# Kernel tuning notes

Hardware: AMD Instinct MI355X
Metric: run time of the kernel (lower is better)

Reference implementation:

```python
import math
import jax, jax.numpy as jnp
import numpy as np

B, C, H, W = 16, 128, 128, 128  # width == dim required by nn.LayerNorm(dim) on (b,c,h,w)
HEADS, DIM_HEAD = 8, 32
INNER = HEADS * DIM_HEAD


def _ln_last(x, g, b, eps=1e-5):
    # torch nn.LayerNorm over the LAST axis (here: width), biased variance
    mu = x.mean(-1, keepdims=True)
    var = x.var(-1, keepdims=True)
    return (x - mu) * jax.lax.rsqrt(var + eps) * g + b


def setup_inputs() -> dict:
    key = jax.random.key(0)
    k0, k1, k2 = jax.random.split(key, 3)
    return {
        "fmap": jax.random.normal(k0, (B, C, H, W), jnp.float32),
        "ln0_g": jnp.ones((C,), jnp.float32),
        "ln0_b": jnp.zeros((C,), jnp.float32),
        "w_qkv": jax.random.normal(k1, (3 * INNER, C), jnp.float32) * 0.05,
        "w_out": jax.random.normal(k2, (C, INNER), jnp.float32) * 0.05,
        "ln1_g": jnp.ones((C,), jnp.float32),
        "ln1_b": jnp.zeros((C,), jnp.float32),
    }


def reference(fmap, ln0_g, ln0_b, w_qkv, w_out, ln1_g, ln1_b):
    b, c, x, y = fmap.shape
    n = x * y
    scale = DIM_HEAD ** -0.5

    fm = _ln_last(fmap, ln0_g, ln0_b)
    # 1x1 conv (no bias) == channel matmul
    qkv = jnp.einsum('bcxy,oc->boxy', fm, w_qkv)  # (b, 3*inner, x, y)
    q, k, v = jnp.split(qkv, 3, axis=1)

    def to_heads(t):
        # b (h c) x y -> (b h) (x y) c
        return t.reshape(b, HEADS, DIM_HEAD, n).transpose(0, 1, 3, 2).reshape(b * HEADS, n, DIM_HEAD)

    q, k, v = map(to_heads, (q, k, v))

    q = jax.nn.softmax(q, axis=-1) * scale
    k = jax.nn.softmax(k, axis=-2)
    # l2norm(v) along feature dim (F.normalize, eps=1e-12)
    v = v / jnp.clip(jnp.linalg.norm(v, axis=-1, keepdims=True), 1e-12)
    inv = 1.0 / math.sqrt(n)
    k = k * inv
    v = v * inv

    context = jnp.einsum('bnd,bne->bde', k, v)   # small (d=32, e=32) context
    out = jnp.einsum('bnd,bde->bne', q, context)

    # (b h) (x y) d -> b (h d) x y
    out = out.reshape(b, HEADS, n, DIM_HEAD).transpose(0, 1, 3, 2).reshape(b, INNER, x, y)
    out = jax.nn.gelu(out, approximate=False)  # torch nn.GELU default (erf)
    out = jnp.einsum('bcxy,oc->boxy', out, w_out)  # 1x1 conv, no bias
    return _ln_last(out, ln1_g, ln1_b)
```

## Files before the change

### kernel.cpp

```cpp
#include <hip/hip_runtime.h>
#include <math.h>

#define OFF_MU    0u
#define OFF_RSTD  262144u
#define OFF_CTXA  655360u
#define OFF_CTXS  2818048u
#define OFF_WSPL  2949120u
#define OFF_WQSPL 3047424u
#define OFF_WOSPL 3096576u

typedef __attribute__((ext_vector_type(8))) short bf16x8;
typedef __attribute__((ext_vector_type(4))) float f32x4;

__global__ void prep_kernel(const float* __restrict__ wqkv,
                            const float* __restrict__ wout,
                            float* __restrict__ ws) {
  int idx = blockIdx.x * 256 + threadIdx.x;
  float v;
  unsigned short* wp;
  unsigned plane, slot;
  if (idx < 65536) {
    int row = idx >> 7, c = idx & 127;
    int blk = row >> 7, ol = row & 127;
    int hh = (ol >> 5) & 1;
    int src = ((ol & 64) ? 512 : 256) + (2 * blk + hh) * 32 + (ol & 31);
    v = wqkv[src * 128 + c];
    wp = (unsigned short*)(ws + OFF_WSPL);
    plane = 65536; slot = (unsigned)idx;
  } else if (idx < 98304) {
    int j = idx - 65536;
    v = wqkv[j];
    wp = (unsigned short*)(ws + OFF_WQSPL);
    plane = 32768; slot = (unsigned)j;
  } else {
    int j = idx - 98304;
    v = wout[j];
    wp = (unsigned short*)(ws + OFF_WOSPL);
    plane = 32768; slot = (unsigned)j;
  }
  unsigned int u = __float_as_uint(v);
  float r1 = v - __uint_as_float(u & 0xffff0000u);
  unsigned int u1 = __float_as_uint(r1);
  float r2 = r1 - __uint_as_float(u1 & 0xffff0000u);
  unsigned int u2 = __float_as_uint(r2);
  wp[slot]             = (unsigned short)(u >> 16);
  wp[plane + slot]     = (unsigned short)(u1 >> 16);
  wp[2 * plane + slot] = (unsigned short)(u2 >> 16);
}

__global__ void ln0_stats_kernel(const float* __restrict__ fmap,
                                 float* __restrict__ ws) {
  const int wid = threadIdx.x >> 6, lane = threadIdx.x & 63;
  const int row = blockIdx.x * 4 + wid;
  const float* p = fmap + (size_t)row * 128;
  float a0 = p[lane], a1 = p[lane + 64];
  double s = (double)a0 + (double)a1;
  double q = (double)a0 * a0 + (double)a1 * a1;
  #pragma unroll
  for (int off = 32; off; off >>= 1) {
    s += __shfl_xor(s, off);
    q += __shfl_xor(q, off);
  }
  if (lane == 0) {
    double mu = s * (1.0 / 128.0);
    double var = q * (1.0 / 128.0) - mu * mu;
    ws[OFF_MU + row] = (float)mu;
    ws[OFF_RSTD + row] = (float)(1.0 / sqrt(var + 1e-5));
  }
}

__launch_bounds__(512, 4)
__global__ void kv_ctx_kernel(const float* __restrict__ fmap,
                              const float* __restrict__ g0,
                              const float* __restrict__ b0,
                              float* __restrict__ ws) {
  __shared__ float sm[13888];
  const int x = blockIdx.x, b = blockIdx.y, t = threadIdx.x;
  const int wave = t >> 6, lane = t & 63;
  const int ln = lane & 15, kb = lane >> 4;
  const int or2 = wave >> 1, yc = wave & 1;
  const int dt = lane >> 3, et = lane & 7;
  const int xg = x >> 3;

  float* pb  = sm;
  float* vb  = sm + 2304;
  float* vss = sm + 4608;
  float* ser = sm + 4864;
  float* rnS = sm + 5120;
  float* red = sm + 5184;
  float* pls = sm + 5184;
  float* muS = sm + 13376;
  float* rsS = sm + 13504;
  float* g0S = sm + 13632;
  float* b0S = sm + 13760;
  float* fmS = sm;

  if (t < 128) {
    muS[t] = ws[OFF_MU + (unsigned)((b * 128 + t) * 128 + x)];
    rsS[t] = ws[OFF_RSTD + (unsigned)((b * 128 + t) * 128 + x)];
  } else if (t < 256) g0S[t - 128] = g0[t - 128];
  else if (t < 384) b0S[t - 256] = b0[t - 256];

  const unsigned short* wspl = (const unsigned short*)(ws + OFF_WSPL);

  for (int blk = 0; blk < 4; ++blk) {
    f32x4 acc[2][4];
    #pragma unroll
    for (int i = 0; i < 2; ++i)
      #pragma unroll
      for (int j = 0; j < 4; ++j) acc[i][j] = (f32x4){0.f, 0.f, 0.f, 0.f};

    for (int cc = 0; cc < 4; ++cc) {
      bf16x8 af[2][3];
      #pragma unroll
      for (int ot = 0; ot < 2; ++ot)
        #pragma unroll
        for (int p = 0; p < 3; ++p)
          af[ot][p] = *(const bf16x8*)(wspl + p * 65536 +
              ((blk * 128 + or2 * 32 + ot * 16 + ln) * 128 + cc * 32 + kb * 8));

      __syncthreads();
      #pragma unroll
      for (int it = 0; it < 2; ++it) {
        int idx4 = it * 512 + t;
        int c = idx4 >> 5, y4 = (idx4 & 31) * 4;
        int cg = cc * 32 + c;
        const float4 r = *(const float4*)(fmap + (((size_t)(b * 128 + cg)) * 128 + x) * 128 + y4);
        float mu = muS[cg], rs = rsS[cg];
        float4 g = *(const float4*)(g0S + y4);
        float4 be = *(const float4*)(b0S + y4);
        float4 o;
        o.x = (r.x - mu) * rs * g.x + be.x;
        o.y = (r.y - mu) * rs * g.y + be.y;
        o.z = (r.z - mu) * rs * g.z + be.z;
        o.w = (r.w - mu) * rs * g.w + be.w;
        *(float4*)(fmS + c * 128 + y4) = o;
      }
      __syncthreads();
      {
        const int ty = t & 127, cg = t >> 7;
        unsigned int d0[4], d1[4], d2[4];
        #pragma unroll
        for (int jj = 0; jj < 4; ++jj) {
          unsigned int h[2], m[2], l[2];
          #pragma unroll
          for (int e = 0; e < 2; ++e) {
            float v = fmS[(cg * 8 + jj * 2 + e) * 128 + ty];
            unsigned int u = __float_as_uint(v);
            float r1 = v - __uint_as_float(u & 0xffff0000u);
            unsigned int u1 = __float_as_uint(r1);
            float r2 = r1 - __uint_as_float(u1 & 0xffff0000u);
            h[e] = u >> 16; m[e] = u1 >> 16; l[e] = __float_as_uint(r2) >> 16;
          }
          d0[jj] = h[0] | (h[1] << 16);
          d1[jj] = m[0] | (m[1] << 16);
          d2[jj] = l[0] | (l[1] << 16);
        }
        float* pp = pls + ty * 20 + cg * 4;
        *reinterpret_cast<uint4*>(pp)        = make_uint4(d0[0], d0[1], d0[2], d0[3]);
        *reinterpret_cast<uint4*>(pp + 2560) = make_uint4(d1[0], d1[1], d1[2], d1[3]);
        *reinterpret_cast<uint4*>(pp + 5120) = make_uint4(d2[0], d2[1], d2[2], d2[3]);
      }
      __syncthreads();
      #pragma unroll
      for (int yt = 0; yt < 4; ++yt) {
        const float* bp = pls + ((yc * 4 + yt) * 16 + ln) * 20 + kb * 4;
        bf16x8 B0 = *(const bf16x8*)(bp);
        bf16x8 B1 = *(const bf16x8*)(bp + 2560);
        bf16x8 B2 = *(const bf16x8*)(bp + 5120);
        #pragma unroll
        for (int ot = 0; ot < 2; ++ot) {
          f32x4 c = acc[ot][yt];
          c = __builtin_amdgcn_mfma_f32_16x16x32_bf16(af[ot][0], B0, c, 0, 0, 0);
          c = __builtin_amdgcn_mfma_f32_16x16x32_bf16(af[ot][0], B1, c, 0, 0, 0);
          c = __builtin_amdgcn_mfma_f32_16x16x32_bf16(af[ot][1], B0, c, 0, 0, 0);
          c = __builtin_amdgcn_mfma_f32_16x16x32_bf16(af[ot][0], B2, c, 0, 0, 0);
          c = __builtin_amdgcn_mfma_f32_16x16x32_bf16(af[ot][1], B1, c, 0, 0, 0);
          c = __builtin_amdgcn_mfma_f32_16x16x32_bf16(af[ot][2], B0, c, 0, 0, 0);
          acc[ot][yt] = c;
        }
      }
    }

    for (int hh = 0; hh < 2; ++hh) {
      float u[16], se[4];
      #pragma unroll
      for (int i = 0; i < 16; ++i) u[i] = 0.0f;
      se[0] = se[1] = se[2] = se[3] = 0.0f;

      for (int hf = 0; hf < 2; ++hf) {
        if (wave == hh * 2 + hf) {
          #pragma unroll
          for (int ot = 0; ot < 2; ++ot)
            #pragma unroll
            for (int yt = 0; yt < 4; ++yt) {
              f32x4 a = acc[ot][yt];
              float4 p;
              p.x = __expf(a[0]); p.y = __expf(a[1]);
              p.z = __expf(a[2]); p.w = __expf(a[3]);
              *(float4*)(pb + (yt * 16 + ln) * 36 + ot * 16 + kb * 4) = p;
            }
        }
        if (wave == 4 + hh * 2 + hf) {
          #pragma unroll
          for (int yt = 0; yt < 4; ++yt) {
            f32x4 a0 = acc[0][yt], a1 = acc[1][yt];
            int yl = yt * 16 + ln;
            *(float4*)(vb + yl * 36 + kb * 4)      = make_float4(a0[0], a0[1], a0[2], a0[3]);
            *(float4*)(vb + yl * 36 + 16 + kb * 4) = make_float4(a1[0], a1[1], a1[2], a1[3]);
            float s = a0[0] * a0[0] + a0[1] * a0[1] + a0[2] * a0[2] + a0[3] * a0[3]
                    + a1[0] * a1[0] + a1[1] * a1[1] + a1[2] * a1[2] + a1[3] * a1[3];
            vss[kb * 64 + yl] = s;
          }
        }
        __syncthreads();
        if (t < 64) {
          float s2 = vss[t] + vss[64 + t] + vss[128 + t] + vss[192 + t];
          rnS[t] = 1.0f / fmaxf(sqrtf(s2), 1e-12f);
        }
        __syncthreads();
        #pragma unroll 2
        for (int yy = 0; yy < 8; ++yy) {
          int y = wave * 8 + yy;
          const float4 p = *(const float4*)(pb + y * 36 + dt * 4);
          float4 v = *(const float4*)(vb + y * 36 + et * 4);
          float rn = rnS[y];
          v.x *= rn; v.y *= rn; v.z *= rn; v.w *= rn;
          se[0] += p.x; se[1] += p.y; se[2] += p.z; se[3] += p.w;
          u[0]  = fmaf(p.x, v.x, u[0]);  u[1]  = fmaf(p.x, v.y, u[1]);
          u[2]  = fmaf(p.x, v.z, u[2]);  u[3]  = fmaf(p.x, v.w, u[3]);
          u[4]  = fmaf(p.y, v.x, u[4]);  u[5]  = fmaf(p.y, v.y, u[5]);
          u[6]  = fmaf(p.y, v.z, u[6]);  u[7]  = fmaf(p.y, v.w, u[7]);
          u[8]  = fmaf(p.z, v.x, u[8]);  u[9]  = fmaf(p.z, v.y, u[9]);
          u[10] = fmaf(p.z, v.z, u[10]); u[11] = fmaf(p.z, v.w, u[11]);
          u[12] = fmaf(p.w, v.x, u[12]); u[13] = fmaf(p.w, v.y, u[13]);
          u[14] = fmaf(p.w, v.z, u[14]); u[15] = fmaf(p.w, v.w, u[15]);
        }
        __syncthreads();
      }
      *(float4*)(red + t * 16 + 0)  = make_float4(u[0], u[1], u[2], u[3]);
      *(float4*)(red + t * 16 + 4)  = make_float4(u[4], u[5], u[6], u[7]);
      *(float4*)(red + t * 16 + 8)  = make_float4(u[8], u[9], u[10], u[11]);
      *(float4*)(red + t * 16 + 12) = make_float4(u[12], u[13], u[14], u[15]);
      if (et == 0)
        *(float4*)(ser + (wave * 8 + dt) * 4) = make_float4(se[0], se[1], se[2], se[3]);
      __syncthreads();
      {
        const int tile = t >> 3;
        const int i0 = (t & 7) * 2;
        float s0 = 0.0f, s1 = 0.0f;
        #pragma unroll
        for (int w = 0; w < 8; ++w) {
          s0 += red[(w * 64 + tile) * 16 + i0];
          s1 += red[(w * 64 + tile) * 16 + i0 + 1];
        }
        const int d = (tile >> 3) * 4 + (i0 >> 2);
        const int e = (tile & 7) * 4 + (i0 & 3);
        float* ca = ws + OFF_CTXA + ((size_t)(b * 8 + blk * 2 + hh) * 16 + xg) * 1056;
        atomicAdd(ca + d * 32 + e, s0);
        atomicAdd(ca + d * 32 + e + 1, s1);
        if (t < 32) {
          float ss = 0.0f;
          #pragma unroll
          for (int w = 0; w < 8; ++w) ss += ser[(w * 8 + (t >> 2)) * 4 + (t & 3)];
          atomicAdd(ca + 1024 + t, ss);
        }
      }
    }
  }
}

__global__ void ctx_reduce_kernel(float* __restrict__ ws) {
  __shared__ float sume[32];
  const int bh = blockIdx.x, t = threadIdx.x;
  const float* ca = ws + OFF_CTXA + (size_t)bh * 16 * 1056;
  if (t < 32) {
    double a = 0.0;
    #pragma unroll
    for (int xg = 0; xg < 16; ++xg) a += ca[xg * 1056 + 1024 + t];
    sume[t] = (float)a;
  }
  __syncthreads();
  const double sb = (1.0 / 16384.0) * 0.17677669529663688;
  #pragma unroll
  for (int i = 0; i < 4; ++i) {
    int de = t + 256 * i;
    double a = 0.0;
    #pragma unroll
    for (int xg = 0; xg < 16; ++xg) a += ca[xg * 1056 + de];
    ws[OFF_CTXS + (size_t)bh * 1024 + de] = (float)(a * sb / (double)sume[de >> 5]);
  }
}

__launch_bounds__(512, 4)
__global__ void final_kernel(const float* __restrict__ fmap,
                             const float* __restrict__ g0,
                             const float* __restrict__ b0,
                             const float* __restrict__ g1,
                             const float* __restrict__ b1,
                             const float* __restrict__ ws,
                             float* __restrict__ out) {
  __shared__ float sm[17792];
  const int x = blockIdx.x, b = blockIdx.y, t = threadIdx.x;
  const int wave = t >> 6, lane = t & 63;
  const int ln = lane & 15, kb = lane >> 4;
  const int or2 = wave >> 1, yc = wave & 1;
  const int yq = t & 127, eg = t >> 7;

  float* fmS = sm;
  float* pls = sm + 4096;
  float* qh  = sm + 11776;
  float* ctxS = sm + 16000;
  float* muS = sm + 17024;
  float* rsS = sm + 17152;
  float* g0S = sm + 17280;
  float* b0S = sm + 17408;
  float* lnm = sm + 17536;
  float* lnr = sm + 17664;

  if (t < 128) {
    muS[t] = ws[OFF_MU + (unsigned)((b * 128 + t) * 128 + x)];
    rsS[t] = ws[OFF_RSTD + (unsigned)((b * 128 + t) * 128 + x)];
  } else if (t < 256) g0S[t - 128] = g0[t - 128];
  else if (t < 384) b0S[t - 256] = b0[t - 256];

  const unsigned short* wqspl = (const unsigned short*)(ws + OFF_WQSPL);
  const unsigned short* wospl = (const unsigned short*)(ws + OFF_WOSPL);

  f32x4 oacc[2][4];
  #pragma unroll
  for (int i = 0; i < 2; ++i)
    #pragma unroll
    for (int j = 0; j < 4; ++j) oacc[i][j] = (f32x4){0.f, 0.f, 0.f, 0.f};

  for (int qblk = 0; qblk < 2; ++qblk) {
    f32x4 qacc[2][4];
    #pragma unroll
    for (int i = 0; i < 2; ++i)
      #pragma unroll
      for (int j = 0; j < 4; ++j) qacc[i][j] = (f32x4){0.f, 0.f, 0.f, 0.f};

    for (int cc = 0; cc < 4; ++cc) {
      bf16x8 af[2][3];
      #pragma unroll
      for (int ot = 0; ot < 2; ++ot)
        #pragma unroll
        for (int p = 0; p < 3; ++p)
          af[ot][p] = *(const bf16x8*)(wqspl + p * 32768 +
              ((qblk * 128 + or2 * 32 + ot * 16 + ln) * 128 + cc * 32 + kb * 8));

      __syncthreads();
      #pragma unroll
      for (int it = 0; it < 2; ++it) {
        int idx4 = it * 512 + t;
        int c = idx4 >> 5, y4 = (idx4 & 31) * 4;
        int cg = cc * 32 + c;
        const float4 r = *(const float4*)(fmap + (((size_t)(b * 128 + cg)) * 128 + x) * 128 + y4);
        float mu = muS[cg], rs = rsS[cg];
        float4 g = *(const float4*)(g0S + y4);
        float4 be = *(const float4*)(b0S + y4);
        float4 o;
        o.x = (r.x - mu) * rs * g.x + be.x;
        o.y = (r.y - mu) * rs * g.y + be.y;
        o.z = (r.z - mu) * rs * g.z + be.z;
        o.w = (r.w - mu) * rs * g.w + be.w;
        *(float4*)(fmS + c * 128 + y4) = o;
      }
      __syncthreads();
      {
        const int ty = t & 127, cg = t >> 7;
        unsigned int d0[4], d1[4], d2[4];
        #pragma unroll
        for (int jj = 0; jj < 4; ++jj) {
          unsigned int h[2], m[2], l[2];
          #pragma unroll
          for (int e = 0; e < 2; ++e) {
            float v = fmS[(cg * 8 + jj * 2 + e) * 128 + ty];
            unsigned int u = __float_as_uint(v);
            float r1 = v - __uint_as_float(u & 0xffff0000u);
            unsigned int u1 = __float_as_uint(r1);
            float r2 = r1 - __uint_as_float(u1 & 0xffff0000u);
            h[e] = u >> 16; m[e] = u1 >> 16; l[e] = __float_as_uint(r2) >> 16;
          }
          d0[jj] = h[0] | (h[1] << 16);
          d1[jj] = m[0] | (m[1] << 16);
          d2[jj] = l[0] | (l[1] << 16);
        }
        float* pp = pls + ty * 20 + cg * 4;
        *reinterpret_cast<uint4*>(pp)        = make_uint4(d0[0], d0[1], d0[2], d0[3]);
        *reinterpret_cast<uint4*>(pp + 2560) = make_uint4(d1[0], d1[1], d1[2], d1[3]);
        *reinterpret_cast<uint4*>(pp + 5120) = make_uint4(d2[0], d2[1], d2[2], d2[3]);
      }
      __syncthreads();
      #pragma unroll
      for (int yt = 0; yt < 4; ++yt) {
        const float* bp = pls + ((yc * 4 + yt) * 16 + ln) * 20 + kb * 4;
        bf16x8 B0 = *(const bf16x8*)(bp);
        bf16x8 B1 = *(const bf16x8*)(bp + 2560);
        bf16x8 B2 = *(const bf16x8*)(bp + 5120);
        #pragma unroll
        for (int ot = 0; ot < 2; ++ot) {
          f32x4 c = qacc[ot][yt];
          c = __builtin_amdgcn_mfma_f32_16x16x32_bf16(af[ot][0], B0, c, 0, 0, 0);
          c = __builtin_amdgcn_mfma_f32_16x16x32_bf16(af[ot][0], B1, c, 0, 0, 0);
          c = __builtin_amdgcn_mfma_f32_16x16x32_bf16(af[ot][1], B0, c, 0, 0, 0);
          c = __builtin_amdgcn_mfma_f32_16x16x32_bf16(af[ot][0], B2, c, 0, 0, 0);
          c = __builtin_amdgcn_mfma_f32_16x16x32_bf16(af[ot][1], B1, c, 0, 0, 0);
          c = __builtin_amdgcn_mfma_f32_16x16x32_bf16(af[ot][2], B0, c, 0, 0, 0);
          qacc[ot][yt] = c;
        }
      }
    }

    for (int hh = 0; hh < 4; ++hh) {
      if (or2 == hh) {
        #pragma unroll
        for (int ot = 0; ot < 2; ++ot)
          #pragma unroll
          for (int yt = 0; yt < 4; ++yt) {
            f32x4 a = qacc[ot][yt];
            int yb = (yc * 4 + yt) * 16 + ln;
            #pragma unroll
            for (int r = 0; r < 4; ++r)
              qh[(ot * 16 + kb * 4 + r) * 132 + yb] = a[r];
          }
      }
      if (t < 256)
        *(float4*)(ctxS + t * 4) =
            *(const float4*)(ws + OFF_CTXS + (size_t)(b * 8 + qblk * 4 + hh) * 1024 + t * 4);
      __syncthreads();
      float ge[8];
      #pragma unroll
      for (int i = 0; i < 8; ++i) ge[i] = 0.0f;
      float ssum = 0.0f;
      #pragma unroll 4
      for (int dd = 0; dd < 32; ++dd) {
        float p = __expf(qh[dd * 132 + yq]);
        ssum += p;
        const float4 c0 = *(const float4*)(ctxS + dd * 32 + eg * 8);
        const float4 c1 = *(const float4*)(ctxS + dd * 32 + eg * 8 + 4);
        ge[0] = fmaf(p, c0.x, ge[0]); ge[1] = fmaf(p, c0.y, ge[1]);
        ge[2] = fmaf(p, c0.z, ge[2]); ge[3] = fmaf(p, c0.w, ge[3]);
        ge[4] = fmaf(p, c1.x, ge[4]); ge[5] = fmaf(p, c1.y, ge[5]);
        ge[6] = fmaf(p, c1.z, ge[6]); ge[7] = fmaf(p, c1.w, ge[7]);
      }
      const float rinv = 1.0f / ssum;
      {
        unsigned int d0[4], d1[4], d2[4];
        #pragma unroll
        for (int j = 0; j < 4; ++j) {
          unsigned int hbt[2], mbt[2], lbt[2];
          #pragma unroll
          for (int e = 0; e < 2; ++e) {
            float v = ge[2 * j + e] * rinv;
            v = 0.5f * v * (1.0f + erff(v * 0.70710678118654752f));
            unsigned int u = __float_as_uint(v);
            float r1 = v - __uint_as_float(u & 0xffff0000u);
            unsigned int u1 = __float_as_uint(r1);
            float r2 = r1 - __uint_as_float(u1 & 0xffff0000u);
            hbt[e] = u >> 16; mbt[e] = u1 >> 16; lbt[e] = __float_as_uint(r2) >> 16;
          }
          d0[j] = hbt[0] | (hbt[1] << 16);
          d1[j] = mbt[0] | (mbt[1] << 16);
          d2[j] = lbt[0] | (lbt[1] << 16);
        }
        float* pp = pls + yq * 20 + eg * 4;
        *reinterpret_cast<uint4*>(pp)        = make_uint4(d0[0], d0[1], d0[2], d0[3]);
        *reinterpret_cast<uint4*>(pp + 2560) = make_uint4(d1[0], d1[1], d1[2], d1[3]);
        *reinterpret_cast<uint4*>(pp + 5120) = make_uint4(d2[0], d2[1], d2[2], d2[3]);
      }
      __syncthreads();
      bf16x8 oaf[2][3];
      #pragma unroll
      for (int ot = 0; ot < 2; ++ot)
        #pragma unroll
        for (int p = 0; p < 3; ++p)
          oaf[ot][p] = *(const bf16x8*)(wospl + p * 32768 +
              ((or2 * 32 + ot * 16 + ln) * 256 + (qblk * 4 + hh) * 32 + kb * 8));
      #pragma unroll
      for (int yt = 0; yt < 4; ++yt) {
        const float* bp = pls + ((yc * 4 + yt) * 16 + ln) * 20 + kb * 4;
        bf16x8 B0 = *(const bf16x8*)(bp);
        bf16x8 B1 = *(const bf16x8*)(bp + 2560);
        bf16x8 B2 = *(const bf16x8*)(bp + 5120);
        #pragma unroll
        for (int ot = 0; ot < 2; ++ot) {
          f32x4 c = oacc[ot][yt];
          c = __builtin_amdgcn_mfma_f32_16x16x32_bf16(oaf[ot][0], B0, c, 0, 0, 0);
          c = __builtin_amdgcn_mfma_f32_16x16x32_bf16(oaf[ot][0], B1, c, 0, 0, 0);
          c = __builtin_amdgcn_mfma_f32_16x16x32_bf16(oaf[ot][1], B0, c, 0, 0, 0);
          c = __builtin_amdgcn_mfma_f32_16x16x32_bf16(oaf[ot][0], B2, c, 0, 0, 0);
          c = __builtin_amdgcn_mfma_f32_16x16x32_bf16(oaf[ot][1], B1, c, 0, 0, 0);
          c = __builtin_amdgcn_mfma_f32_16x16x32_bf16(oaf[ot][2], B0, c, 0, 0, 0);
          oacc[ot][yt] = c;
        }
      }
    }
  }

  __syncthreads();
  float* red_s = sm;
  float* red_q = sm + 4096;
  #pragma unroll
  for (int ot = 0; ot < 2; ++ot)
    #pragma unroll
    for (int r = 0; r < 4; ++r) {
      int o = or2 * 32 + ot * 16 + kb * 4 + r;
      float s = 0.0f, q = 0.0f;
      #pragma unroll
      for (int yt = 0; yt < 4; ++yt) { float v = oacc[ot][yt][r]; s += v; q = fmaf(v, v, q); }
      red_s[o * 32 + yc * 16 + ln] = s;
      red_q[o * 32 + yc * 16 + ln] = q;
    }
  __syncthreads();
  if (t < 128) {
    double s = 0.0, q = 0.0;
    #pragma unroll
    for (int i = 0; i < 32; ++i) { s += red_s[t * 32 + i]; q += red_q[t * 32 + i]; }
    double mu = s * (1.0 / 128.0);
    double var = q * (1.0 / 128.0) - mu * mu;
    lnm[t] = (float)mu;
    lnr[t] = (float)(1.0 / sqrt(var + 1e-5));
  }
  __syncthreads();
  float g1v[4], b1v[4];
  #pragma unroll
  for (int yt = 0; yt < 4; ++yt) {
    int y = (yc * 4 + yt) * 16 + ln;
    g1v[yt] = g1[y]; b1v[yt] = b1[y];
  }
  #pragma unroll
  for (int ot = 0; ot < 2; ++ot)
    #pragma unroll
    for (int r = 0; r < 4; ++r) {
      int o = or2 * 32 + ot * 16 + kb * 4 + r;
      float mu = lnm[o], rs = lnr[o];
      #pragma unroll
      for (int yt = 0; yt < 4; ++yt) {
        int y = (yc * 4 + yt) * 16 + ln;
        out[(((size_t)(b * 128 + o)) * 128 + x) * 128 + y] =
            (oacc[ot][yt][r] - mu) * rs * g1v[yt] + b1v[yt];
      }
    }
}

extern "C" void kernel_launch(void* const* d_in, const int* in_sizes, int n_in,
                              void* d_out, int out_size, void* d_ws, size_t ws_size,
                              hipStream_t stream) {
  const float* fmap = (const float*)d_in[0];
  const float* g0   = (const float*)d_in[1];
  const float* b0   = (const float*)d_in[2];
  const float* wqkv = (const float*)d_in[3];
  const float* wout = (const float*)d_in[4];
  const float* g1   = (const float*)d_in[5];
  const float* b1   = (const float*)d_in[6];
  float* ws  = (float*)d_ws;
  float* out = (float*)d_out;

  hipMemsetAsync((char*)d_ws + (size_t)OFF_CTXA * 4, 0, (size_t)2162688 * 4, stream);
  prep_kernel<<<512, 256, 0, stream>>>(wqkv, wout, ws);
  ln0_stats_kernel<<<65536, 256, 0, stream>>>(fmap, ws);
  kv_ctx_kernel<<<dim3(128, 16), 512, 0, stream>>>(fmap, g0, b0, ws);
  ctx_reduce_kernel<<<128, 256, 0, stream>>>(ws);
  final_kernel<<<dim3(128, 16), 512, 0, stream>>>(fmap, g0, b0, g1, b1, ws, out);
}
```

Baseline: 1.055 ms.

## Compute q-softmax times context with split-bf16 MFMA in registers

The scalar per-head loop in the final kernel, which staged q in shared memory and did exp plus FMA against a shared-memory context, is replaced. Each wave now exponentiates its q accumulators in registers, reduces the softmax denominators with cross-lane shuffles, and multiplies by the context using three-way bf16-split MFMAs. The context reduce kernel writes the context pre-split and permuted into MFMA operand order, and the w_out weights are permuted to match. GELU output is staged through a smaller shared buffer in two phases that each cover two heads, which cuts barriers and shared-memory use. The risks are mismatched permutations and higher register pressure.

```diff
diff --git a/kernel.cpp b/kernel.cpp
--- a/kernel.cpp
+++ b/kernel.cpp
@@ -3,14 +3,34 @@
 
 #define OFF_MU    0u
 #define OFF_RSTD  262144u
-#define OFF_CTXA  655360u
-#define OFF_CTXS  2818048u
-#define OFF_WSPL  2949120u
-#define OFF_WQSPL 3047424u
-#define OFF_WOSPL 3096576u
+#define OFF_CTXA  524288u
+#define OFF_CTXP  2686976u
+#define OFF_WSPL  2883584u
+#define OFF_WQSPL 2981888u
+#define OFF_WOSPL 3031040u
 
 typedef __attribute__((ext_vector_type(8))) short bf16x8;
 typedef __attribute__((ext_vector_type(4))) float f32x4;
+
+__device__ __forceinline__ void split3(float v, unsigned& h, unsigned& m, unsigned& l) {
+  unsigned u = __float_as_uint(v);
+  float r1 = v - __uint_as_float(u & 0xffff0000u);
+  unsigned u1 = __float_as_uint(r1);
+  float r2 = r1 - __uint_as_float(u1 & 0xffff0000u);
+  h = u >> 16; m = u1 >> 16; l = __float_as_uint(r2) >> 16;
+}
+
+__device__ __forceinline__ f32x4 mfma6(const bf16x8& A0, const bf16x8& A1, const bf16x8& A2,
+                                       const bf16x8& B0, const bf16x8& B1, const bf16x8& B2,
+                                       f32x4 c) {
+  c = __builtin_amdgcn_mfma_f32_16x16x32_bf16(A0, B0, c, 0, 0, 0);
+  c = __builtin_amdgcn_mfma_f32_16x16x32_bf16(A0, B1, c, 0, 0, 0);
+  c = __builtin_amdgcn_mfma_f32_16x16x32_bf16(A1, B0, c, 0, 0, 0);
+  c = __builtin_amdgcn_mfma_f32_16x16x32_bf16(A0, B2, c, 0, 0, 0);
+  c = __builtin_amdgcn_mfma_f32_16x16x32_bf16(A1, B1, c, 0, 0, 0);
+  c = __builtin_amdgcn_mfma_f32_16x16x32_bf16(A2, B0, c, 0, 0, 0);
+  return c;
+}
 
 __global__ void prep_kernel(const float* __restrict__ wqkv,
                             const float* __restrict__ wout,
@@ -34,18 +54,17 @@
     plane = 32768; slot = (unsigned)j;
   } else {
     int j = idx - 98304;
-    v = wout[j];
+    int o = j >> 8, k = j & 255;
+    int cp = (k & 0xE0) | (((k >> 2) & 1) << 4) | (((k >> 3) & 3) << 2) | (k & 3);
+    v = wout[o * 256 + cp];
     wp = (unsigned short*)(ws + OFF_WOSPL);
     plane = 32768; slot = (unsigned)j;
   }
-  unsigned int u = __float_as_uint(v);
-  float r1 = v - __uint_as_float(u & 0xffff0000u);
-  unsigned int u1 = __float_as_uint(r1);
-  float r2 = r1 - __uint_as_float(u1 & 0xffff0000u);
-  unsigned int u2 = __float_as_uint(r2);
-  wp[slot]             = (unsigned short)(u >> 16);
-  wp[plane + slot]     = (unsigned short)(u1 >> 16);
-  wp[2 * plane + slot] = (unsigned short)(u2 >> 16);
+  unsigned h, m, l;
+  split3(v, h, m, l);
+  wp[slot]             = (unsigned short)h;
+  wp[plane + slot]     = (unsigned short)m;
+  wp[2 * plane + slot] = (unsigned short)l;
 }
 
 __global__ void ln0_stats_kernel(const float* __restrict__ fmap,
@@ -146,11 +165,7 @@
           #pragma unroll
           for (int e = 0; e < 2; ++e) {
             float v = fmS[(cg * 8 + jj * 2 + e) * 128 + ty];
-            unsigned int u = __float_as_uint(v);
-            float r1 = v - __uint_as_float(u & 0xffff0000u);
-            unsigned int u1 = __float_as_uint(r1);
-            float r2 = r1 - __uint_as_float(u1 & 0xffff0000u);
-            h[e] = u >> 16; m[e] = u1 >> 16; l[e] = __float_as_uint(r2) >> 16;
+            split3(v, h[e], m[e], l[e]);
           }
           d0[jj] = h[0] | (h[1] << 16);
           d1[jj] = m[0] | (m[1] << 16);
@@ -169,16 +184,8 @@
         bf16x8 B1 = *(const bf16x8*)(bp + 2560);
         bf16x8 B2 = *(const bf16x8*)(bp + 5120);
         #pragma unroll
-        for (int ot = 0; ot < 2; ++ot) {
-          f32x4 c = acc[ot][yt];
-          c = __builtin_amdgcn_mfma_f32_16x16x32_bf16(af[ot][0], B0, c, 0, 0, 0);
-          c = __builtin_amdgcn_mfma_f32_16x16x32_bf16(af[ot][0], B1, c, 0, 0, 0);
-          c = __builtin_amdgcn_mfma_f32_16x16x32_bf16(af[ot][1], B0, c, 0, 0, 0);
-          c = __builtin_amdgcn_mfma_f32_16x16x32_bf16(af[ot][0], B2, c, 0, 0, 0);
-          c = __builtin_amdgcn_mfma_f32_16x16x32_bf16(af[ot][1], B1, c, 0, 0, 0);
-          c = __builtin_amdgcn_mfma_f32_16x16x32_bf16(af[ot][2], B0, c, 0, 0, 0);
-          acc[ot][yt] = c;
-        }
+        for (int ot = 0; ot < 2; ++ot)
+          acc[ot][yt] = mfma6(af[ot][0], af[ot][1], af[ot][2], B0, B1, B2, acc[ot][yt]);
       }
     }
 
@@ -282,13 +289,21 @@
   }
   __syncthreads();
   const double sb = (1.0 / 16384.0) * 0.17677669529663688;
+  unsigned short* cp = (unsigned short*)(ws + OFF_CTXP) + (size_t)bh * 3072;
   #pragma unroll
   for (int i = 0; i < 4; ++i) {
     int de = t + 256 * i;
+    int d = de >> 5, e = de & 31;
     double a = 0.0;
     #pragma unroll
     for (int xg = 0; xg < 16; ++xg) a += ca[xg * 1056 + de];
-    ws[OFF_CTXS + (size_t)bh * 1024 + de] = (float)(a * sb / (double)sume[de >> 5]);
+    float v = (float)(a * sb / (double)sume[d]);
+    int k = ((d >> 2) & 3) * 8 + ((d >> 4) & 1) * 4 + (d & 3);
+    unsigned h, m, l;
+    split3(v, h, m, l);
+    cp[e * 32 + k]        = (unsigned short)h;
+    cp[1024 + e * 32 + k] = (unsigned short)m;
+    cp[2048 + e * 32 + k] = (unsigned short)l;
   }
 }
 
@@ -300,23 +315,21 @@
                              const float* __restrict__ b1,
                              const float* __restrict__ ws,
                              float* __restrict__ out) {
-  __shared__ float sm[17792];
+  __shared__ float sm[14592];
   const int x = blockIdx.x, b = blockIdx.y, t = threadIdx.x;
   const int wave = t >> 6, lane = t & 63;
   const int ln = lane & 15, kb = lane >> 4;
   const int or2 = wave >> 1, yc = wave & 1;
-  const int yq = t & 127, eg = t >> 7;
 
   float* fmS = sm;
   float* pls = sm + 4096;
-  float* qh  = sm + 11776;
-  float* ctxS = sm + 16000;
-  float* muS = sm + 17024;
-  float* rsS = sm + 17152;
-  float* g0S = sm + 17280;
-  float* b0S = sm + 17408;
-  float* lnm = sm + 17536;
-  float* lnr = sm + 17664;
+  float* gel = sm;
+  float* muS = sm + 13824;
+  float* rsS = sm + 13952;
+  float* g0S = sm + 14080;
+  float* b0S = sm + 14208;
+  float* lnm = sm + 14336;
+  float* lnr = sm + 14464;
 
   if (t < 128) {
     muS[t] = ws[OFF_MU + (unsigned)((b * 128 + t) * 128 + x)];
@@ -326,6 +339,7 @@
 
   const unsigned short* wqspl = (const unsigned short*)(ws + OFF_WQSPL);
   const unsigned short* wospl = (const unsigned short*)(ws + OFF_WOSPL);
+  const unsigned short* ctxp  = (const unsigned short*)(ws + OFF_CTXP);
 
   f32x4 oacc[2][4];
   #pragma unroll
@@ -376,11 +390,7 @@
           #pragma unroll
           for (int e = 0; e < 2; ++e) {
             float v = fmS[(cg * 8 + jj * 2 + e) * 128 + ty];
-            unsigned int u = __float_as_uint(v);
-            float r1 = v - __uint_as_float(u & 0xffff0000u);
-            unsigned int u1 = __float_as_uint(r1);
-            float r2 = r1 - __uint_as_float(u1 & 0xffff0000u);
-            h[e] = u >> 16; m[e] = u1 >> 16; l[e] = __float_as_uint(r2) >> 16;
+            split3(v, h[e], m[e], l[e]);
           }
           d0[jj] = h[0] | (h[1] << 16);
           d1[jj] = m[0] | (m[1] << 16);
@@ -399,100 +409,106 @@
         bf16x8 B1 = *(const bf16x8*)(bp + 2560);
         bf16x8 B2 = *(const bf16x8*)(bp + 5120);
         #pragma unroll
-        for (int ot = 0; ot < 2; ++ot) {
-          f32x4 c = qacc[ot][yt];
-          c = __builtin_amdgcn_mfma_f32_16x16x32_bf16(af[ot][0], B0, c, 0, 0, 0);
-          c = __builtin_amdgcn_mfma_f32_16x16x32_bf16(af[ot][0], B1, c, 0, 0, 0);
-          c = __builtin_amdgcn_mfma_f32_16x16x32_bf16(af[ot][1], B0, c, 0, 0, 0);
-          c = __builtin_amdgcn_mfma_f32_16x16x32_bf16(af[ot][0], B2, c, 0, 0, 0);
-          c = __builtin_amdgcn_mfma_f32_16x16x32_bf16(af[ot][1], B1, c, 0, 0, 0);
-          c = __builtin_amdgcn_mfma_f32_16x16x32_bf16(af[ot][2], B0, c, 0, 0, 0);
-          qacc[ot][yt] = c;
-        }
-      }
-    }
-
-    for (int hh = 0; hh < 4; ++hh) {
-      if (or2 == hh) {
-        #pragma unroll
         for (int ot = 0; ot < 2; ++ot)
-          #pragma unroll
-          for (int yt = 0; yt < 4; ++yt) {
-            f32x4 a = qacc[ot][yt];
-            int yb = (yc * 4 + yt) * 16 + ln;
-            #pragma unroll
-            for (int r = 0; r < 4; ++r)
-              qh[(ot * 16 + kb * 4 + r) * 132 + yb] = a[r];
+          qacc[ot][yt] = mfma6(af[ot][0], af[ot][1], af[ot][2], B0, B1, B2, qacc[ot][yt]);
+      }
+    }
+
+    float rssum[4];
+    bf16x8 pf0[4], pf1[4], pf2[4];
+    #pragma unroll
+    for (int yt = 0; yt < 4; ++yt) {
+      float pv[8];
+      #pragma unroll
+      for (int ot = 0; ot < 2; ++ot)
+        #pragma unroll
+        for (int r = 0; r < 4; ++r)
+          pv[ot * 4 + r] = __expf(qacc[ot][yt][r]);
+      float ps = ((pv[0] + pv[1]) + (pv[2] + pv[3])) + ((pv[4] + pv[5]) + (pv[6] + pv[7]));
+      ps += __shfl_xor(ps, 16);
+      ps += __shfl_xor(ps, 32);
+      rssum[yt] = 1.0f / ps;
+      unsigned wh[4], wm[4], wl[4];
+      #pragma unroll
+      for (int j = 0; j < 4; ++j) {
+        unsigned h0, m0, l0, h1, m1, l1;
+        split3(pv[2 * j], h0, m0, l0);
+        split3(pv[2 * j + 1], h1, m1, l1);
+        wh[j] = h0 | (h1 << 16);
+        wm[j] = m0 | (m1 << 16);
+        wl[j] = l0 | (l1 << 16);
+      }
+      uint4 uh = make_uint4(wh[0], wh[1], wh[2], wh[3]);
+      uint4 um = make_uint4(wm[0], wm[1], wm[2], wm[3]);
+      uint4 ul = make_uint4(wl[0], wl[1], wl[2], wl[3]);
+      pf0[yt] = *(const bf16x8*)&uh;
+      pf1[yt] = *(const bf16x8*)&um;
+      pf2[yt] = *(const bf16x8*)&ul;
+    }
+
+    f32x4 ge[2][4];
+    const unsigned short* chp = ctxp + (size_t)(b * 8 + qblk * 4 + or2) * 3072;
+    #pragma unroll
+    for (int ot = 0; ot < 2; ++ot) {
+      bf16x8 aq0 = *(const bf16x8*)(chp +        (ot * 16 + ln) * 32 + kb * 8);
+      bf16x8 aq1 = *(const bf16x8*)(chp + 1024 + (ot * 16 + ln) * 32 + kb * 8);
+      bf16x8 aq2 = *(const bf16x8*)(chp + 2048 + (ot * 16 + ln) * 32 + kb * 8);
+      #pragma unroll
+      for (int yt = 0; yt < 4; ++yt) {
+        f32x4 c = (f32x4){0.f, 0.f, 0.f, 0.f};
+        ge[ot][yt] = mfma6(aq0, aq1, aq2, pf0[yt], pf1[yt], pf2[yt], c);
+      }
+    }
+
+    #pragma unroll
+    for (int ot = 0; ot < 2; ++ot)
+      #pragma unroll
+      for (int yt = 0; yt < 4; ++yt)
+        #pragma unroll
+        for (int r = 0; r < 4; ++r) {
+          float v = ge[ot][yt][r] * rssum[yt];
+          ge[ot][yt][r] = 0.5f * v * (1.0f + erff(v * 0.70710678118654752f));
+        }
+
+    for (int ph = 0; ph < 2; ++ph) {
+      __syncthreads();
+      if ((or2 >> 1) == ph) {
+        const int c16 = (or2 & 1) * 16;
+        #pragma unroll
+        for (int yt = 0; yt < 4; ++yt) {
+          float* grow = gel + ((yc * 4 + yt) * 16 + ln) * 36 + c16 + kb * 4;
+          #pragma unroll
+          for (int ot = 0; ot < 2; ++ot) {
+            unsigned h0, m0, l0, h1, m1, l1, h2, m2, l2, h3, m3, l3;
+            split3(ge[ot][yt][0], h0, m0, l0);
+            split3(ge[ot][yt][1], h1, m1, l1);
+            split3(ge[ot][yt][2], h2, m2, l2);
+            split3(ge[ot][yt][3], h3, m3, l3);
+            *(uint2*)(grow + ot * 2)        = make_uint2(h0 | (h1 << 16), h2 | (h3 << 16));
+            *(uint2*)(grow + 4608 + ot * 2) = make_uint2(m0 | (m1 << 16), m2 | (m3 << 16));
+            *(uint2*)(grow + 9216 + ot * 2) = make_uint2(l0 | (l1 << 16), l2 | (l3 << 16));
           }
-      }
-      if (t < 256)
-        *(float4*)(ctxS + t * 4) =
-            *(const float4*)(ws + OFF_CTXS + (size_t)(b * 8 + qblk * 4 + hh) * 1024 + t * 4);
-      __syncthreads();
-      float ge[8];
-      #pragma unroll
-      for (int i = 0; i < 8; ++i) ge[i] = 0.0f;
-      float ssum = 0.0f;
-      #pragma unroll 4
-      for (int dd = 0; dd < 32; ++dd) {
-        float p = __expf(qh[dd * 132 + yq]);
-        ssum += p;
-        const float4 c0 = *(const float4*)(ctxS + dd * 32 + eg * 8);
-        const float4 c1 = *(const float4*)(ctxS + dd * 32 + eg * 8 + 4);
-        ge[0] = fmaf(p, c0.x, ge[0]); ge[1] = fmaf(p, c0.y, ge[1]);
-        ge[2] = fmaf(p, c0.z, ge[2]); ge[3] = fmaf(p, c0.w, ge[3]);
-        ge[4] = fmaf(p, c1.x, ge[4]); ge[5] = fmaf(p, c1.y, ge[5]);
-        ge[6] = fmaf(p, c1.z, ge[6]); ge[7] = fmaf(p, c1.w, ge[7]);
-      }
-      const float rinv = 1.0f / ssum;
-      {
-        unsigned int d0[4], d1[4], d2[4];
-        #pragma unroll
-        for (int j = 0; j < 4; ++j) {
-          unsigned int hbt[2], mbt[2], lbt[2];
-          #pragma unroll
-          for (int e = 0; e < 2; ++e) {
-            float v = ge[2 * j + e] * rinv;
-            v = 0.5f * v * (1.0f + erff(v * 0.70710678118654752f));
-            unsigned int u = __float_as_uint(v);
-            float r1 = v - __uint_as_float(u & 0xffff0000u);
-            unsigned int u1 = __float_as_uint(r1);
-            float r2 = r1 - __uint_as_float(u1 & 0xffff0000u);
-            hbt[e] = u >> 16; mbt[e] = u1 >> 16; lbt[e] = __float_as_uint(r2) >> 16;
-          }
-          d0[j] = hbt[0] | (hbt[1] << 16);
-          d1[j] = mbt[0] | (mbt[1] << 16);
-          d2[j] = lbt[0] | (lbt[1] << 16);
-        }
-        float* pp = pls + yq * 20 + eg * 4;
-        *reinterpret_cast<uint4*>(pp)        = make_uint4(d0[0], d0[1], d0[2], d0[3]);
-        *reinterpret_cast<uint4*>(pp + 2560) = make_uint4(d1[0], d1[1], d1[2], d1[3]);
-        *reinterpret_cast<uint4*>(pp + 5120) = make_uint4(d2[0], d2[1], d2[2], d2[3]);
-      }
-      __syncthreads();
-      bf16x8 oaf[2][3];
-      #pragma unroll
-      for (int ot = 0; ot < 2; ++ot)
-        #pragma unroll
-        for (int p = 0; p < 3; ++p)
-          oaf[ot][p] = *(const bf16x8*)(wospl + p * 32768 +
-              ((or2 * 32 + ot * 16 + ln) * 256 + (qblk * 4 + hh) * 32 + kb * 8));
-      #pragma unroll
-      for (int yt = 0; yt < 4; ++yt) {
-        const float* bp = pls + ((yc * 4 + yt) * 16 + ln) * 20 + kb * 4;
-        bf16x8 B0 = *(const bf16x8*)(bp);
-        bf16x8 B1 = *(const bf16x8*)(bp + 2560);
-        bf16x8 B2 = *(const bf16x8*)(bp + 5120);
-        #pragma unroll
-        for (int ot = 0; ot < 2; ++ot) {
-          f32x4 c = oacc[ot][yt];
-          c = __builtin_amdgcn_mfma_f32_16x16x32_bf16(oaf[ot][0], B0, c, 0, 0, 0);
-          c = __builtin_amdgcn_mfma_f32_16x16x32_bf16(oaf[ot][0], B1, c, 0, 0, 0);
-          c = __builtin_amdgcn_mfma_f32_16x16x32_bf16(oaf[ot][1], B0, c, 0, 0, 0);
-          c = __builtin_amdgcn_mfma_f32_16x16x32_bf16(oaf[ot][0], B2, c, 0, 0, 0);
-          c = __builtin_amdgcn_mfma_f32_16x16x32_bf16(oaf[ot][1], B1, c, 0, 0, 0);
-          c = __builtin_amdgcn_mfma_f32_16x16x32_bf16(oaf[ot][2], B0, c, 0, 0, 0);
-          oacc[ot][yt] = c;
+        }
+      }
+      __syncthreads();
+      #pragma unroll
+      for (int kc = 0; kc < 2; ++kc) {
+        bf16x8 ao[2][3];
+        #pragma unroll
+        for (int ot = 0; ot < 2; ++ot)
+          #pragma unroll
+          for (int p = 0; p < 3; ++p)
+            ao[ot][p] = *(const bf16x8*)(wospl + p * 32768 +
+                ((or2 * 32 + ot * 16 + ln) * 256 + qblk * 128 + ph * 64 + kc * 32 + kb * 8));
+        #pragma unroll
+        for (int yt = 0; yt < 4; ++yt) {
+          const float* bp = gel + ((yc * 4 + yt) * 16 + ln) * 36 + kc * 16 + kb * 4;
+          bf16x8 B0 = *(const bf16x8*)(bp);
+          bf16x8 B1 = *(const bf16x8*)(bp + 4608);
+          bf16x8 B2 = *(const bf16x8*)(bp + 9216);
+          #pragma unroll
+          for (int ot = 0; ot < 2; ++ot)
+            oacc[ot][yt] = mfma6(ao[ot][0], ao[ot][1], ao[ot][2], B0, B1, B2, oacc[ot][yt]);
         }
       }
     }
```

New measurement: 1.043 ms. Within noise of the previous version (-1.1%).
